# Kernel tuning notes

Hardware: AMD Instinct MI355X
Metric: run time of the kernel (lower is better)

The kernel has to match this reference:

```python
import jax, jax.numpy as jnp
import numpy as np

N = 50000      # num_nodes
E = 800000     # num_edges (avg degree 16)
D = 128        # embedding_dim
HID = 32       # per-head hidden dim of conv1
H = 8          # heads of conv1
OUT = 128      # output_dim


def setup_inputs() -> dict:
    key = jax.random.key(0)
    ks = jax.random.split(key, 14)
    s = lambda fan_in: 1.0 / np.sqrt(fan_in)
    return {
        "x": jax.random.randint(ks[0], (N,), 0, N),
        "edge_index": jax.random.randint(ks[1], (2, E), 0, N),
        "emb": jax.random.normal(ks[2], (N, D), jnp.float32),
        # conv1: GATConv(D, HID, heads=H, concat=True)
        "W1": jax.random.normal(ks[3], (D, H * HID), jnp.float32) * s(D),
        "a_src1": jax.random.normal(ks[4], (H, HID), jnp.float32) * s(HID),
        "a_dst1": jax.random.normal(ks[5], (H, HID), jnp.float32) * s(HID),
        "b1": jnp.zeros((H * HID,), jnp.float32),
        # conv2: GATConv(H*HID, OUT, heads=1, concat=False)
        "W2": jax.random.normal(ks[6], (H * HID, OUT), jnp.float32) * s(H * HID),
        "a_src2": jax.random.normal(ks[7], (1, OUT), jnp.float32) * s(OUT),
        "a_dst2": jax.random.normal(ks[8], (1, OUT), jnp.float32) * s(OUT),
        "b2": jnp.zeros((OUT,), jnp.float32),
        # output Linear(OUT, OUT)
        "Wo": jax.random.normal(ks[9], (OUT, OUT), jnp.float32) * s(OUT),
        "bo": jnp.zeros((OUT,), jnp.float32),
    }


def _segment_softmax(e, seg, n):
    # e: [E, H]; softmax over edges sharing the same destination node
    m = jax.ops.segment_max(e, seg, num_segments=n)            # [N, H]
    ex = jnp.exp(e - m[seg])
    denom = jax.ops.segment_sum(ex, seg, num_segments=n)       # [N, H]
    return ex / (denom[seg] + 1e-16)


def _gat_conv(x, src, dst, W, a_src, a_dst, b, concat):
    n = x.shape[0]
    Hh, C = a_src.shape
    h = (x @ W).reshape(n, Hh, C)                              # [N, H, C]
    al_src = (h * a_src).sum(-1)                               # [N, H]
    al_dst = (h * a_dst).sum(-1)                               # [N, H]
    e = jax.nn.leaky_relu(al_src[src] + al_dst[dst], 0.2)      # [E, H]
    alpha = _segment_softmax(e, dst, n)                        # [E, H]
    out = jax.ops.segment_sum(h[src] * alpha[:, :, None], dst, num_segments=n)
    out = out.reshape(n, Hh * C) if concat else out.mean(axis=1)
    return out + b


def reference(x, edge_index, emb, W1, a_src1, a_dst1, b1,
              W2, a_src2, a_dst2, b2, Wo, bo):
    n = x.shape[0]
    loops = jnp.arange(n)
    src = jnp.concatenate([edge_index[0], loops])              # add self-loops (PyG default)
    dst = jnp.concatenate([edge_index[1], loops])
    h = emb[x]                                                 # [N, D]
    h = _gat_conv(h, src, dst, W1, a_src1, a_dst1, b1, concat=True)
    h = _gat_conv(h, src, dst, W2, a_src2, a_dst2, b2, concat=False)
    return h @ Wo + bo
```

## Files before the change

kernel.cpp:

```cpp
#include <hip/hip_runtime.h>
#include <hip/hip_bf16.h>

#define NN 50000
#define EE 800000
#define DD 128
#define F1 256
#define F2 128

using short8  = __attribute__((ext_vector_type(8))) short;
using floatx4 = __attribute__((ext_vector_type(4))) float;

__device__ inline float bf2f(ushort u) { return __uint_as_float(((unsigned)u) << 16); }
__device__ inline ushort f2bf(float f) {
    unsigned u = __float_as_uint(f);
    u += 0x7fffu + ((u >> 16) & 1u);
    return (ushort)(u >> 16);
}

#define HB ((EE + 255) / 256)
#define W1B ((DD * F1 + 255) / 256)
#define W2B ((F1 * F2 + 255) / 256)
#define WOB ((F2 * F2 + 255) / 256)

__global__ __launch_bounds__(256) void k_prep(
    const int* __restrict__ edst, int* __restrict__ cnt,
    const float* __restrict__ W1, ushort* __restrict__ W1t,
    const float* __restrict__ W2, ushort* __restrict__ W2t,
    const float* __restrict__ Wo, ushort* __restrict__ Wot,
    const float* __restrict__ b2, const float* __restrict__ bo,
    float* __restrict__ bc) {
    int b = blockIdx.x;
    if (b < HB) {
        int i = b * 256 + threadIdx.x;
        if (i < EE) atomicAdd(&cnt[edst[i]], 1);
    } else if (b < HB + W1B) {
        int idx = (b - HB) * 256 + threadIdx.x;
        int k = idx / F1, n = idx % F1;
        W1t[(size_t)n * DD + k] = f2bf(W1[(size_t)k * F1 + n]);
    } else if (b < HB + W1B + W2B) {
        int idx = (b - HB - W1B) * 256 + threadIdx.x;
        int k = idx / F2, n = idx % F2;
        W2t[(size_t)n * F1 + k] = f2bf(W2[(size_t)k * F2 + n]);
    } else if (b < HB + W1B + W2B + WOB) {
        int idx = (b - HB - W1B - W2B) * 256 + threadIdx.x;
        int k = idx / F2, n = idx % F2;
        Wot[(size_t)n * F2 + k] = f2bf(Wo[(size_t)k * F2 + n]);
    } else {
        int j = threadIdx.x;
        if (j < F2) {
            float s = bo[j];
            for (int k = 0; k < F2; ++k) s += b2[k] * Wo[(size_t)k * F2 + j];
            bc[j] = s;
        }
    }
}

__global__ void k_scan1(const int* __restrict__ cnt, int* __restrict__ out,
                        int* __restrict__ sums) {
    __shared__ int s[256];
    int i = blockIdx.x * 256 + threadIdx.x;
    int v = (i < NN) ? cnt[i] + 1 : 0;
    s[threadIdx.x] = v;
    __syncthreads();
    for (int off = 1; off < 256; off <<= 1) {
        int t = (threadIdx.x >= off) ? s[threadIdx.x - off] : 0;
        __syncthreads();
        s[threadIdx.x] += t;
        __syncthreads();
    }
    if (i < NN) out[i] = s[threadIdx.x] - v;
    if (threadIdx.x == 255) sums[blockIdx.x] = s[255];
}

__global__ void k_scan3(int* __restrict__ offsets, const int* __restrict__ sums,
                        int* __restrict__ cursor, int nb) {
    __shared__ int s[256];
    int v = (threadIdx.x < nb) ? sums[threadIdx.x] : 0;
    s[threadIdx.x] = v;
    __syncthreads();
    for (int off = 1; off < 256; off <<= 1) {
        int t = (threadIdx.x >= off) ? s[threadIdx.x - off] : 0;
        __syncthreads();
        s[threadIdx.x] += t;
        __syncthreads();
    }
    int base = (blockIdx.x == 0) ? 0 : s[blockIdx.x - 1];
    int i = blockIdx.x * 256 + threadIdx.x;
    if (i < NN) {
        int o = offsets[i] + base;
        offsets[i] = o;
        cursor[i] = o;
    }
    if (blockIdx.x == 0 && threadIdx.x == 0) offsets[NN] = EE + NN;
}

__global__ void k_scatter(const int* __restrict__ esrc, const int* __restrict__ edst,
                          const int* __restrict__ offsets,
                          int* __restrict__ cursor, int* __restrict__ srcs) {
    int i = blockIdx.x * 256 + threadIdx.x;
    if (i < EE) {
        int pos = atomicAdd(&cursor[edst[i]], 1);
        srcs[pos] = esrc[i];
    } else if (i < EE + NN) {
        int n = i - EE;
        srcs[offsets[n + 1] - 1] = n;
    }
}

__global__ __launch_bounds__(256, 2) void k_gemm1(
    const int* __restrict__ x, const float* __restrict__ emb,
    const ushort* __restrict__ Bt,
    ushort* __restrict__ Cout,
    const float* __restrict__ avs, const float* __restrict__ avd,
    float* __restrict__ out_s, float* __restrict__ out_d) {
    __shared__ ushort As[128][72];
    __shared__ ushort Bs[128][72];
    const int t    = threadIdx.x;
    const int lane = t & 63;
    const int w    = t >> 6;
    const int wr   = w >> 1, wc = w & 1;
    const int m0   = blockIdx.x * 128;
    const int n0   = blockIdx.y * 128;
    floatx4 acc[4][4] = {};
    for (int k0 = 0; k0 < DD; k0 += 64) {
        #pragma unroll
        for (int p = 0; p < 4; ++p) {
            int linear = p * 2048 + t * 8;
            int row = linear >> 6;
            int col = linear & 63;
            short8 va = {};
            int gm = m0 + row;
            if (gm < NN) {
                const float* er = emb + (size_t)x[gm] * DD + k0 + col;
                float4 f0 = *(const float4*)er;
                float4 f1 = *(const float4*)(er + 4);
                va[0] = f2bf(f0.x); va[1] = f2bf(f0.y);
                va[2] = f2bf(f0.z); va[3] = f2bf(f0.w);
                va[4] = f2bf(f1.x); va[5] = f2bf(f1.y);
                va[6] = f2bf(f1.z); va[7] = f2bf(f1.w);
            }
            *(short8*)&As[row][col] = va;
            short8 vb = *(const short8*)(Bt + (size_t)(n0 + row) * DD + k0 + col);
            *(short8*)&Bs[row][col] = vb;
        }
        __syncthreads();
        #pragma unroll
        for (int kk = 0; kk < 64; kk += 32) {
            const int q8 = (lane >> 4) * 8;
            short8 af[4], bf[4];
            #pragma unroll
            for (int i = 0; i < 4; ++i)
                af[i] = *(const short8*)&As[wr * 64 + i * 16 + (lane & 15)][kk + q8];
            #pragma unroll
            for (int j = 0; j < 4; ++j)
                bf[j] = *(const short8*)&Bs[wc * 64 + j * 16 + (lane & 15)][kk + q8];
            #pragma unroll
            for (int i = 0; i < 4; ++i)
                #pragma unroll
                for (int j = 0; j < 4; ++j)
                    acc[i][j] = __builtin_amdgcn_mfma_f32_16x16x32_bf16(
                        af[i], bf[j], acc[i][j], 0, 0, 0);
        }
        __syncthreads();
    }
    const int r0 = (lane >> 4) * 4;
    const int cc = lane & 15;
    float as0 = avs[n0 + wc * 64 +  0 + cc], ad0 = avd[n0 + wc * 64 +  0 + cc];
    float as1 = avs[n0 + wc * 64 + 16 + cc], ad1 = avd[n0 + wc * 64 + 16 + cc];
    float as2 = avs[n0 + wc * 64 + 32 + cc], ad2 = avd[n0 + wc * 64 + 32 + cc];
    float as3 = avs[n0 + wc * 64 + 48 + cc], ad3 = avd[n0 + wc * 64 + 48 + cc];
    #pragma unroll
    for (int i = 0; i < 4; ++i) {
        #pragma unroll
        for (int r = 0; r < 4; ++r) {
            int m = m0 + wr * 64 + i * 16 + r0 + r;
            float hs0 = acc[i][0][r] * as0 + acc[i][1][r] * as1;
            float hs1 = acc[i][2][r] * as2 + acc[i][3][r] * as3;
            float hd0 = acc[i][0][r] * ad0 + acc[i][1][r] * ad1;
            float hd1 = acc[i][2][r] * ad2 + acc[i][3][r] * ad3;
            #pragma unroll
            for (int mask = 1; mask < 16; mask <<= 1) {
                hs0 += __shfl_xor(hs0, mask);
                hs1 += __shfl_xor(hs1, mask);
                hd0 += __shfl_xor(hd0, mask);
                hd1 += __shfl_xor(hd1, mask);
            }
            if (cc == 0 && m < NN) {
                int gh = (n0 >> 5) + wc * 2;
                out_s[m * 8 + gh] = hs0;   out_s[m * 8 + gh + 1] = hs1;
                out_d[m * 8 + gh] = hd0;   out_d[m * 8 + gh + 1] = hd1;
            }
            if (m < NN) {
                #pragma unroll
                for (int j = 0; j < 4; ++j)
                    Cout[(size_t)m * F1 + n0 + wc * 64 + j * 16 + cc] = f2bf(acc[i][j][r]);
            }
        }
    }
}

__global__ __launch_bounds__(256, 2) void k_gemm23(
    const ushort* __restrict__ A,
    const ushort* __restrict__ Bt,
    const ushort* __restrict__ Wot,
    ushort* __restrict__ h3,
    const float* __restrict__ avs, const float* __restrict__ avd,
    float* __restrict__ out_s, float* __restrict__ out_d) {
    __shared__ __align__(16) char smem[69632];
    ushort (*As)[72]   = (ushort(*)[72])smem;
    ushort (*Bs)[72]   = (ushort(*)[72])(smem + 18432);
    ushort (*h2t)[136] = (ushort(*)[136])smem;
    ushort (*Wt)[136]  = (ushort(*)[136])(smem + 34816);
    __shared__ float als[2][128], ald[2][128];
    const int t    = threadIdx.x;
    const int lane = t & 63;
    const int w    = t >> 6;
    const int wr   = w >> 1, wc = w & 1;
    const int m0   = blockIdx.x * 128;
    floatx4 acc[4][4] = {};
    for (int k0 = 0; k0 < F1; k0 += 64) {
        #pragma unroll
        for (int p = 0; p < 4; ++p) {
            int linear = p * 2048 + t * 8;
            int row = linear >> 6;
            int col = linear & 63;
            short8 va = {};
            int gm = m0 + row;
            if (gm < NN) va = *(const short8*)(A + (size_t)gm * F1 + k0 + col);
            *(short8*)&As[row][col] = va;
            short8 vb = *(const short8*)(Bt + (size_t)row * F1 + k0 + col);
            *(short8*)&Bs[row][col] = vb;
        }
        __syncthreads();
        #pragma unroll
        for (int kk = 0; kk < 64; kk += 32) {
            const int q8 = (lane >> 4) * 8;
            short8 af[4], bf[4];
            #pragma unroll
            for (int i = 0; i < 4; ++i)
                af[i] = *(const short8*)&As[wr * 64 + i * 16 + (lane & 15)][kk + q8];
            #pragma unroll
            for (int j = 0; j < 4; ++j)
                bf[j] = *(const short8*)&Bs[wc * 64 + j * 16 + (lane & 15)][kk + q8];
            #pragma unroll
            for (int i = 0; i < 4; ++i)
                #pragma unroll
                for (int j = 0; j < 4; ++j)
                    acc[i][j] = __builtin_amdgcn_mfma_f32_16x16x32_bf16(
                        af[i], bf[j], acc[i][j], 0, 0, 0);
        }
        __syncthreads();
    }
    const int r0 = (lane >> 4) * 4;
    const int cc = lane & 15;
    {
        float as0 = avs[wc * 64 +  0 + cc], ad0 = avd[wc * 64 +  0 + cc];
        float as1 = avs[wc * 64 + 16 + cc], ad1 = avd[wc * 64 + 16 + cc];
        float as2 = avs[wc * 64 + 32 + cc], ad2 = avd[wc * 64 + 32 + cc];
        float as3 = avs[wc * 64 + 48 + cc], ad3 = avd[wc * 64 + 48 + cc];
        #pragma unroll
        for (int i = 0; i < 4; ++i) {
            #pragma unroll
            for (int r = 0; r < 4; ++r) {
                float ps = acc[i][0][r] * as0 + acc[i][1][r] * as1
                         + acc[i][2][r] * as2 + acc[i][3][r] * as3;
                float pd = acc[i][0][r] * ad0 + acc[i][1][r] * ad1
                         + acc[i][2][r] * ad2 + acc[i][3][r] * ad3;
                #pragma unroll
                for (int mask = 1; mask < 16; mask <<= 1) {
                    ps += __shfl_xor(ps, mask);
                    pd += __shfl_xor(pd, mask);
                }
                if (cc == 0) {
                    int lr = wr * 64 + i * 16 + r0 + r;
                    als[wc][lr] = ps;
                    ald[wc][lr] = pd;
                }
            }
        }
    }
    #pragma unroll
    for (int i = 0; i < 4; ++i)
        #pragma unroll
        for (int r = 0; r < 4; ++r)
            #pragma unroll
            for (int j = 0; j < 4; ++j)
                h2t[wr * 64 + i * 16 + r0 + r][wc * 64 + j * 16 + cc] = f2bf(acc[i][j][r]);
    #pragma unroll
    for (int p = 0; p < 8; ++p) {
        int linear = p * 2048 + t * 8;
        int row = linear >> 7;
        int col = linear & 127;
        *(short8*)&Wt[row][col] = *(const short8*)(Wot + (size_t)row * F2 + col);
    }
    __syncthreads();
    if (t < 128) {
        int m = m0 + t;
        if (m < NN) {
            out_s[m] = als[0][t] + als[1][t];
            out_d[m] = ald[0][t] + ald[1][t];
        }
    }
    floatx4 acc2[4][4] = {};
    #pragma unroll
    for (int kk = 0; kk < 128; kk += 32) {
        const int q8 = (lane >> 4) * 8;
        short8 af[4], bf[4];
        #pragma unroll
        for (int i = 0; i < 4; ++i)
            af[i] = *(const short8*)&h2t[wr * 64 + i * 16 + (lane & 15)][kk + q8];
        #pragma unroll
        for (int j = 0; j < 4; ++j)
            bf[j] = *(const short8*)&Wt[wc * 64 + j * 16 + (lane & 15)][kk + q8];
        #pragma unroll
        for (int i = 0; i < 4; ++i)
            #pragma unroll
            for (int j = 0; j < 4; ++j)
                acc2[i][j] = __builtin_amdgcn_mfma_f32_16x16x32_bf16(
                    af[i], bf[j], acc2[i][j], 0, 0, 0);
    }
    #pragma unroll
    for (int i = 0; i < 4; ++i) {
        #pragma unroll
        for (int r = 0; r < 4; ++r) {
            int m = m0 + wr * 64 + i * 16 + r0 + r;
            if (m < NN) {
                #pragma unroll
                for (int j = 0; j < 4; ++j)
                    h3[(size_t)m * F2 + wc * 64 + j * 16 + cc] = f2bf(acc2[i][j][r]);
            }
        }
    }
}

__device__ inline float lrelu(float x) { return x > 0.f ? x : 0.2f * x; }

__global__ __launch_bounds__(256) void k_agg1(
    const int* __restrict__ offsets, const int* __restrict__ srcs,
    const ushort* __restrict__ h1, const float* __restrict__ a1s,
    const float* __restrict__ a1d, const float* __restrict__ b1,
    ushort* __restrict__ out1) {
    __shared__ float atab[4][512];
    __shared__ int   stab[4][64];
    const int w = threadIdx.x >> 6;
    const int d = blockIdx.x * 4 + w;
    if (d >= NN) return;
    const int lane = threadIdx.x & 63;
    const int beg = offsets[d], end = offsets[d + 1];
    const int deg = end - beg;
    const int e8 = lane >> 3, h8 = lane & 7;
    const float ad = a1d[d * 8 + h8];
    const int hh = lane >> 3;
    float4 acc = make_float4(0.f, 0.f, 0.f, 0.f);

    if (deg <= 64) {
        float m = -1e30f, den = 0.f;
        for (int e = e8; e < deg; e += 8) {
            int s = srcs[beg + e];
            if (h8 == 0) stab[w][e] = s;
            float v = lrelu(a1s[s * 8 + h8] + ad);
            atab[w][e * 8 + h8] = v;
            float nm = fmaxf(m, v);
            den = den * __expf(m - nm) + __expf(v - nm);
            m = nm;
        }
        #pragma unroll
        for (int mask = 8; mask < 64; mask <<= 1) {
            float om = __shfl_xor(m, mask);
            float od = __shfl_xor(den, mask);
            float nm = fmaxf(m, om);
            den = den * __expf(m - nm) + od * __expf(om - nm);
            m = nm;
        }
        float rden = 1.f / (den + 1e-16f);
        for (int p = lane; p < deg * 8; p += 64)
            atab[w][p] = __expf(atab[w][p] - m) * rden;
        int e = 0;
        for (; e + 8 <= deg; e += 8) {
            ushort4 u[8]; float a[8];
            #pragma unroll
            for (int jj = 0; jj < 8; ++jj) {
                int s = stab[w][e + jj];
                u[jj] = *(const ushort4*)(h1 + (size_t)s * F1 + lane * 4);
                a[jj] = atab[w][(e + jj) * 8 + hh];
            }
            #pragma unroll
            for (int jj = 0; jj < 8; ++jj) {
                acc.x += a[jj] * bf2f(u[jj].x);
                acc.y += a[jj] * bf2f(u[jj].y);
                acc.z += a[jj] * bf2f(u[jj].z);
                acc.w += a[jj] * bf2f(u[jj].w);
            }
        }
        for (; e < deg; ++e) {
            int s = stab[w][e];
            float alpha = atab[w][e * 8 + hh];
            ushort4 u = *(const ushort4*)(h1 + (size_t)s * F1 + lane * 4);
            acc.x += alpha * bf2f(u.x); acc.y += alpha * bf2f(u.y);
            acc.z += alpha * bf2f(u.z); acc.w += alpha * bf2f(u.w);
        }
    } else {
        float m = -1e30f, den = 0.f;
        for (int i = beg + e8; i < end; i += 8) {
            int s = srcs[i];
            float v = lrelu(a1s[s * 8 + h8] + ad);
            float nm = fmaxf(m, v);
            den = den * __expf(m - nm) + __expf(v - nm);
            m = nm;
        }
        #pragma unroll
        for (int mask = 8; mask < 64; mask <<= 1) {
            float om = __shfl_xor(m, mask);
            float od = __shfl_xor(den, mask);
            float nm = fmaxf(m, om);
            den = den * __expf(m - nm) + od * __expf(om - nm);
            m = nm;
        }
        float rden = 1.f / (den + 1e-16f);
        for (int tb = beg; tb < end; tb += 64) {
            int cnt = min(64, end - tb);
            if (lane < cnt) stab[w][lane] = srcs[tb + lane];
            int np = cnt * 8;
            for (int p = lane; p < np; p += 64) {
                int s = stab[w][p >> 3];
                float v = lrelu(a1s[s * 8 + h8] + ad);
                atab[w][p] = __expf(v - m) * rden;
            }
            for (int e = 0; e < cnt; ++e) {
                int s = stab[w][e];
                float alpha = atab[w][e * 8 + hh];
                ushort4 u = *(const ushort4*)(h1 + (size_t)s * F1 + lane * 4);
                acc.x += alpha * bf2f(u.x); acc.y += alpha * bf2f(u.y);
                acc.z += alpha * bf2f(u.z); acc.w += alpha * bf2f(u.w);
            }
        }
    }
    float4 bb = *(const float4*)(b1 + lane * 4);
    ushort4 o;
    o.x = f2bf(acc.x + bb.x); o.y = f2bf(acc.y + bb.y);
    o.z = f2bf(acc.z + bb.z); o.w = f2bf(acc.w + bb.w);
    *(ushort4*)(out1 + (size_t)d * F1 + lane * 4) = o;
}

__global__ __launch_bounds__(256) void k_agg2(
    const int* __restrict__ offsets, const int* __restrict__ srcs,
    const ushort* __restrict__ h3, const float* __restrict__ a2s,
    const float* __restrict__ a2d, const float* __restrict__ bc,
    float* __restrict__ out) {
    __shared__ float atab[4][64];
    __shared__ int   stab[4][64];
    const int w = threadIdx.x >> 6;
    const int d = blockIdx.x * 4 + w;
    if (d >= NN) return;
    const int lane = threadIdx.x & 63;
    const int beg = offsets[d], end = offsets[d + 1];
    const int deg = end - beg;
    const float ad = a2d[d];
    float2 acc = make_float2(0.f, 0.f);

    if (deg <= 64) {
        float m = -1e30f, den = 0.f;
        if (lane < deg) {
            int s = srcs[beg + lane];
            stab[w][lane] = s;
            float v = lrelu(a2s[s] + ad);
            atab[w][lane] = v;
            m = v;
            den = 1.f;
        }
        #pragma unroll
        for (int mask = 1; mask < 64; mask <<= 1) {
            float om = __shfl_xor(m, mask);
            float od = __shfl_xor(den, mask);
            float nm = fmaxf(m, om);
            den = den * __expf(m - nm) + od * __expf(om - nm);
            m = nm;
        }
        float rden = 1.f / (den + 1e-16f);
        if (lane < deg)
            atab[w][lane] = __expf(atab[w][lane] - m) * rden;
        int e = 0;
        for (; e + 8 <= deg; e += 8) {
            ushort2 u[8]; float a[8];
            #pragma unroll
            for (int jj = 0; jj < 8; ++jj) {
                int s = stab[w][e + jj];
                u[jj] = *(const ushort2*)(h3 + (size_t)s * F2 + lane * 2);
                a[jj] = atab[w][e + jj];
            }
            #pragma unroll
            for (int jj = 0; jj < 8; ++jj) {
                acc.x += a[jj] * bf2f(u[jj].x);
                acc.y += a[jj] * bf2f(u[jj].y);
            }
        }
        for (; e < deg; ++e) {
            int s = stab[w][e];
            float alpha = atab[w][e];
            ushort2 u = *(const ushort2*)(h3 + (size_t)s * F2 + lane * 2);
            acc.x += alpha * bf2f(u.x); acc.y += alpha * bf2f(u.y);
        }
    } else {
        float m = -1e30f, den = 0.f;
        for (int i = beg + lane; i < end; i += 64) {
            int s = srcs[i];
            float v = lrelu(a2s[s] + ad);
            float nm = fmaxf(m, v);
            den = den * __expf(m - nm) + __expf(v - nm);
            m = nm;
        }
        #pragma unroll
        for (int mask = 1; mask < 64; mask <<= 1) {
            float om = __shfl_xor(m, mask);
            float od = __shfl_xor(den, mask);
            float nm = fmaxf(m, om);
            den = den * __expf(m - nm) + od * __expf(om - nm);
            m = nm;
        }
        float rden = 1.f / (den + 1e-16f);
        for (int tb = beg; tb < end; tb += 64) {
            int cnt = min(64, end - tb);
            if (lane < cnt) {
                int s = srcs[tb + lane];
                stab[w][lane] = s;
                atab[w][lane] = __expf(lrelu(a2s[s] + ad) - m) * rden;
            }
            for (int e = 0; e < cnt; ++e) {
                int s = stab[w][e];
                float alpha = atab[w][e];
                ushort2 u = *(const ushort2*)(h3 + (size_t)s * F2 + lane * 2);
                acc.x += alpha * bf2f(u.x); acc.y += alpha * bf2f(u.y);
            }
        }
    }
    float2 bb = *(const float2*)(bc + lane * 2);
    *(float2*)(out + (size_t)d * F2 + lane * 2) = make_float2(acc.x + bb.x, acc.y + bb.y);
}

extern "C" void kernel_launch(void* const* d_in, const int* in_sizes, int n_in,
                              void* d_out, int out_size, void* d_ws, size_t ws_size,
                              hipStream_t stream) {
    const int*   x      = (const int*)d_in[0];
    const int*   edge   = (const int*)d_in[1];
    const float* emb    = (const float*)d_in[2];
    const float* W1     = (const float*)d_in[3];
    const float* a_src1 = (const float*)d_in[4];
    const float* a_dst1 = (const float*)d_in[5];
    const float* b1     = (const float*)d_in[6];
    const float* W2     = (const float*)d_in[7];
    const float* a_src2 = (const float*)d_in[8];
    const float* a_dst2 = (const float*)d_in[9];
    const float* b2     = (const float*)d_in[10];
    const float* Wo     = (const float*)d_in[11];
    const float* bo     = (const float*)d_in[12];
    float* out = (float*)d_out;

    char* w = (char*)d_ws;
    auto alloc = [&](size_t bytes) {
        char* p = w;
        w += (bytes + 255) & ~(size_t)255;
        return p;
    };
    int*    offsets = (int*)alloc((NN + 1) * sizeof(int));
    int*    cursor  = (int*)alloc(NN * sizeof(int));
    int*    sums    = (int*)alloc(256 * sizeof(int));
    int*    srcs    = (int*)alloc((size_t)(EE + NN) * sizeof(int));
    ushort* W1t     = (ushort*)alloc((size_t)DD * F1 * sizeof(ushort));
    ushort* W2t     = (ushort*)alloc((size_t)F1 * F2 * sizeof(ushort));
    ushort* Wot     = (ushort*)alloc((size_t)F2 * F2 * sizeof(ushort));
    ushort* h1      = (ushort*)alloc((size_t)NN * F1 * sizeof(ushort));
    ushort* out1    = (ushort*)alloc((size_t)NN * F1 * sizeof(ushort));
    ushort* h3      = (ushort*)alloc((size_t)NN * F2 * sizeof(ushort));
    float*  a1s     = (float*)alloc((size_t)NN * 8 * sizeof(float));
    float*  a1d     = (float*)alloc((size_t)NN * 8 * sizeof(float));
    float*  bc      = (float*)alloc(F2 * sizeof(float));
    float*  a2s     = a1s;
    float*  a2d     = a1d;

    const int* esrc = edge;
    const int* edst = edge + EE;

    const int NB = (NN + 255) / 256;

    hipMemsetAsync(cursor, 0, NN * sizeof(int), stream);
    k_prep<<<HB + W1B + W2B + WOB + 1, 256, 0, stream>>>(
        edst, cursor, W1, W1t, W2, W2t, Wo, Wot, b2, bo, bc);
    k_scan1<<<NB, 256, 0, stream>>>(cursor, offsets, sums);
    k_scan3<<<NB, 256, 0, stream>>>(offsets, sums, cursor, NB);
    k_scatter<<<(EE + NN + 255) / 256, 256, 0, stream>>>(esrc, edst, offsets, cursor, srcs);

    const int MT = (NN + 127) / 128;

    k_gemm1<<<dim3(MT, F1 / 128), 256, 0, stream>>>(
        x, emb, W1t, h1, a_src1, a_dst1, a1s, a1d);
    k_agg1<<<(NN + 3) / 4, 256, 0, stream>>>(offsets, srcs, h1, a1s, a1d, b1, out1);

    k_gemm23<<<dim3(MT, 1), 256, 0, stream>>>(
        out1, W2t, Wot, h3, a_src2, a_dst2, a2s, a2d);

    k_agg2<<<(NN + 3) / 4, 256, 0, stream>>>(offsets, srcs, h3, a2s, a2d, bc, out);
}
```

Baseline: 346.9 us.

## Fuse CSR build into cooperative kernel and use half-wave per node in aggregation

Replaces the memset plus the four preprocessing kernels (count, two scan passes, scatter) with a single cooperative kernel of 256 blocks that separates the phases with grid-wide syncs. This removes several launches and the memset, but the atomic count and scatter phases now run on only 256 blocks with grid-stride loops, where they used to run on thousands. Both aggregation kernels now give each destination node 32 lanes instead of a full 64-lane wavefront, with wider per-lane vector loads (8 bf16 in agg1, 4 in agg2) and 8 nodes per block. This is meant to cut idle lanes on low-degree nodes and raise memory-level parallelism for the gathers.

```diff
diff --git a/kernel.cpp b/kernel.cpp
--- a/kernel.cpp
+++ b/kernel.cpp
@@ -1,11 +1,15 @@
 #include <hip/hip_runtime.h>
 #include <hip/hip_bf16.h>
+#include <hip/hip_cooperative_groups.h>
+
+namespace cg = cooperative_groups;
 
 #define NN 50000
 #define EE 800000
 #define DD 128
 #define F1 256
 #define F2 128
+#define NB196 196
 
 using short8  = __attribute__((ext_vector_type(8))) short;
 using floatx4 = __attribute__((ext_vector_type(4))) float;
@@ -17,94 +21,87 @@
     return (ushort)(u >> 16);
 }
 
-#define HB ((EE + 255) / 256)
-#define W1B ((DD * F1 + 255) / 256)
-#define W2B ((F1 * F2 + 255) / 256)
-#define WOB ((F2 * F2 + 255) / 256)
-
-__global__ __launch_bounds__(256) void k_prep(
-    const int* __restrict__ edst, int* __restrict__ cnt,
+__global__ __launch_bounds__(256) void k_build(
+    const int* __restrict__ esrc, const int* __restrict__ edst,
+    int* __restrict__ cnt,
+    int* __restrict__ offsets, int* __restrict__ sums, int* __restrict__ srcs,
     const float* __restrict__ W1, ushort* __restrict__ W1t,
     const float* __restrict__ W2, ushort* __restrict__ W2t,
     const float* __restrict__ Wo, ushort* __restrict__ Wot,
     const float* __restrict__ b2, const float* __restrict__ bo,
     float* __restrict__ bc) {
-    int b = blockIdx.x;
-    if (b < HB) {
-        int i = b * 256 + threadIdx.x;
-        if (i < EE) atomicAdd(&cnt[edst[i]], 1);
-    } else if (b < HB + W1B) {
-        int idx = (b - HB) * 256 + threadIdx.x;
-        int k = idx / F1, n = idx % F1;
+    cg::grid_group grid = cg::this_grid();
+    const int tid = blockIdx.x * 256 + threadIdx.x;
+    const int NT  = gridDim.x * 256;
+    __shared__ int s[256];
+
+    for (int i = tid; i < NN; i += NT) cnt[i] = 0;
+    grid.sync();
+
+    for (int i = tid; i < EE; i += NT) atomicAdd(&cnt[edst[i]], 1);
+    for (int i = tid; i < DD * F1; i += NT) {
+        int k = i / F1, n = i % F1;
         W1t[(size_t)n * DD + k] = f2bf(W1[(size_t)k * F1 + n]);
-    } else if (b < HB + W1B + W2B) {
-        int idx = (b - HB - W1B) * 256 + threadIdx.x;
-        int k = idx / F2, n = idx % F2;
+    }
+    for (int i = tid; i < F1 * F2; i += NT) {
+        int k = i / F2, n = i % F2;
         W2t[(size_t)n * F1 + k] = f2bf(W2[(size_t)k * F2 + n]);
-    } else if (b < HB + W1B + W2B + WOB) {
-        int idx = (b - HB - W1B - W2B) * 256 + threadIdx.x;
-        int k = idx / F2, n = idx % F2;
+    }
+    for (int i = tid; i < F2 * F2; i += NT) {
+        int k = i / F2, n = i % F2;
         Wot[(size_t)n * F2 + k] = f2bf(Wo[(size_t)k * F2 + n]);
-    } else {
-        int j = threadIdx.x;
-        if (j < F2) {
-            float s = bo[j];
-            for (int k = 0; k < F2; ++k) s += b2[k] * Wo[(size_t)k * F2 + j];
-            bc[j] = s;
-        }
-    }
-}
-
-__global__ void k_scan1(const int* __restrict__ cnt, int* __restrict__ out,
-                        int* __restrict__ sums) {
-    __shared__ int s[256];
-    int i = blockIdx.x * 256 + threadIdx.x;
-    int v = (i < NN) ? cnt[i] + 1 : 0;
-    s[threadIdx.x] = v;
-    __syncthreads();
-    for (int off = 1; off < 256; off <<= 1) {
-        int t = (threadIdx.x >= off) ? s[threadIdx.x - off] : 0;
+    }
+    if (tid < F2) {
+        float acc = bo[tid];
+        for (int k = 0; k < F2; ++k) acc += b2[k] * Wo[(size_t)k * F2 + tid];
+        bc[tid] = acc;
+    }
+    grid.sync();
+
+    if (blockIdx.x < NB196) {
+        int i = blockIdx.x * 256 + threadIdx.x;
+        int v = (i < NN) ? cnt[i] + 1 : 0;
+        s[threadIdx.x] = v;
         __syncthreads();
-        s[threadIdx.x] += t;
+        for (int off = 1; off < 256; off <<= 1) {
+            int t2 = (threadIdx.x >= off) ? s[threadIdx.x - off] : 0;
+            __syncthreads();
+            s[threadIdx.x] += t2;
+            __syncthreads();
+        }
+        if (i < NN) offsets[i] = s[threadIdx.x] - v;
+        if (threadIdx.x == 255) sums[blockIdx.x] = s[255];
+    }
+    grid.sync();
+
+    {
+        int v = (threadIdx.x < NB196) ? sums[threadIdx.x] : 0;
+        s[threadIdx.x] = v;
         __syncthreads();
-    }
-    if (i < NN) out[i] = s[threadIdx.x] - v;
-    if (threadIdx.x == 255) sums[blockIdx.x] = s[255];
-}
-
-__global__ void k_scan3(int* __restrict__ offsets, const int* __restrict__ sums,
-                        int* __restrict__ cursor, int nb) {
-    __shared__ int s[256];
-    int v = (threadIdx.x < nb) ? sums[threadIdx.x] : 0;
-    s[threadIdx.x] = v;
-    __syncthreads();
-    for (int off = 1; off < 256; off <<= 1) {
-        int t = (threadIdx.x >= off) ? s[threadIdx.x - off] : 0;
-        __syncthreads();
-        s[threadIdx.x] += t;
-        __syncthreads();
-    }
-    int base = (blockIdx.x == 0) ? 0 : s[blockIdx.x - 1];
-    int i = blockIdx.x * 256 + threadIdx.x;
-    if (i < NN) {
-        int o = offsets[i] + base;
-        offsets[i] = o;
-        cursor[i] = o;
-    }
-    if (blockIdx.x == 0 && threadIdx.x == 0) offsets[NN] = EE + NN;
-}
-
-__global__ void k_scatter(const int* __restrict__ esrc, const int* __restrict__ edst,
-                          const int* __restrict__ offsets,
-                          int* __restrict__ cursor, int* __restrict__ srcs) {
-    int i = blockIdx.x * 256 + threadIdx.x;
-    if (i < EE) {
-        int pos = atomicAdd(&cursor[edst[i]], 1);
+        for (int off = 1; off < 256; off <<= 1) {
+            int t2 = (threadIdx.x >= off) ? s[threadIdx.x - off] : 0;
+            __syncthreads();
+            s[threadIdx.x] += t2;
+            __syncthreads();
+        }
+        if (blockIdx.x < NB196) {
+            int base = (blockIdx.x == 0) ? 0 : s[blockIdx.x - 1];
+            int i = blockIdx.x * 256 + threadIdx.x;
+            if (i < NN) {
+                int o = offsets[i] + base;
+                offsets[i] = o;
+                cnt[i] = o;
+            }
+        }
+        if (blockIdx.x == 0 && threadIdx.x == 0) offsets[NN] = EE + NN;
+    }
+    grid.sync();
+
+    for (int i = tid; i < EE; i += NT) {
+        int pos = atomicAdd(&cnt[edst[i]], 1);
         srcs[pos] = esrc[i];
-    } else if (i < EE + NN) {
-        int n = i - EE;
-        srcs[offsets[n + 1] - 1] = n;
-    }
+    }
+    for (int i = tid; i < NN; i += NT) srcs[offsets[i + 1] - 1] = i;
 }
 
 __global__ __launch_bounds__(256, 2) void k_gemm1(
@@ -340,32 +337,32 @@
     const ushort* __restrict__ h1, const float* __restrict__ a1s,
     const float* __restrict__ a1d, const float* __restrict__ b1,
     ushort* __restrict__ out1) {
-    __shared__ float atab[4][512];
-    __shared__ int   stab[4][64];
-    const int w = threadIdx.x >> 6;
-    const int d = blockIdx.x * 4 + w;
+    __shared__ float atab[8][512];
+    __shared__ int   stab[8][64];
+    const int hw = threadIdx.x >> 5;
+    const int d  = blockIdx.x * 8 + hw;
     if (d >= NN) return;
-    const int lane = threadIdx.x & 63;
+    const int l   = threadIdx.x & 31;
     const int beg = offsets[d], end = offsets[d + 1];
     const int deg = end - beg;
-    const int e8 = lane >> 3, h8 = lane & 7;
+    const int e4 = l >> 3, h8 = l & 7;
     const float ad = a1d[d * 8 + h8];
-    const int hh = lane >> 3;
-    float4 acc = make_float4(0.f, 0.f, 0.f, 0.f);
+    const int hh = l >> 2;
+    float accv[8] = {};
 
     if (deg <= 64) {
         float m = -1e30f, den = 0.f;
-        for (int e = e8; e < deg; e += 8) {
+        for (int e = e4; e < deg; e += 4) {
             int s = srcs[beg + e];
-            if (h8 == 0) stab[w][e] = s;
+            if (h8 == 0) stab[hw][e] = s;
             float v = lrelu(a1s[s * 8 + h8] + ad);
-            atab[w][e * 8 + h8] = v;
+            atab[hw][e * 8 + h8] = v;
             float nm = fmaxf(m, v);
             den = den * __expf(m - nm) + __expf(v - nm);
             m = nm;
         }
         #pragma unroll
-        for (int mask = 8; mask < 64; mask <<= 1) {
+        for (int mask = 8; mask < 32; mask <<= 1) {
             float om = __shfl_xor(m, mask);
             float od = __shfl_xor(den, mask);
             float nm = fmaxf(m, om);
@@ -373,35 +370,34 @@
             m = nm;
         }
         float rden = 1.f / (den + 1e-16f);
-        for (int p = lane; p < deg * 8; p += 64)
-            atab[w][p] = __expf(atab[w][p] - m) * rden;
+        for (int p = l; p < deg * 8; p += 32)
+            atab[hw][p] = __expf(atab[hw][p] - m) * rden;
         int e = 0;
-        for (; e + 8 <= deg; e += 8) {
-            ushort4 u[8]; float a[8];
-            #pragma unroll
-            for (int jj = 0; jj < 8; ++jj) {
-                int s = stab[w][e + jj];
-                u[jj] = *(const ushort4*)(h1 + (size_t)s * F1 + lane * 4);
-                a[jj] = atab[w][(e + jj) * 8 + hh];
-            }
-            #pragma unroll
-            for (int jj = 0; jj < 8; ++jj) {
-                acc.x += a[jj] * bf2f(u[jj].x);
-                acc.y += a[jj] * bf2f(u[jj].y);
-                acc.z += a[jj] * bf2f(u[jj].z);
-                acc.w += a[jj] * bf2f(u[jj].w);
-            }
+        for (; e + 4 <= deg; e += 4) {
+            short8 u[4]; float a[4];
+            #pragma unroll
+            for (int jj = 0; jj < 4; ++jj) {
+                int s = stab[hw][e + jj];
+                u[jj] = *(const short8*)(h1 + (size_t)s * F1 + l * 8);
+                a[jj] = atab[hw][(e + jj) * 8 + hh];
+            }
+            #pragma unroll
+            for (int jj = 0; jj < 4; ++jj)
+                #pragma unroll
+                for (int c = 0; c < 8; ++c)
+                    accv[c] += a[jj] * bf2f((ushort)u[jj][c]);
         }
         for (; e < deg; ++e) {
-            int s = stab[w][e];
-            float alpha = atab[w][e * 8 + hh];
-            ushort4 u = *(const ushort4*)(h1 + (size_t)s * F1 + lane * 4);
-            acc.x += alpha * bf2f(u.x); acc.y += alpha * bf2f(u.y);
-            acc.z += alpha * bf2f(u.z); acc.w += alpha * bf2f(u.w);
+            int s = stab[hw][e];
+            float alpha = atab[hw][e * 8 + hh];
+            short8 u = *(const short8*)(h1 + (size_t)s * F1 + l * 8);
+            #pragma unroll
+            for (int c = 0; c < 8; ++c)
+                accv[c] += alpha * bf2f((ushort)u[c]);
         }
     } else {
         float m = -1e30f, den = 0.f;
-        for (int i = beg + e8; i < end; i += 8) {
+        for (int i = beg + e4; i < end; i += 4) {
             int s = srcs[i];
             float v = lrelu(a1s[s * 8 + h8] + ad);
             float nm = fmaxf(m, v);
@@ -409,7 +405,7 @@
             m = nm;
         }
         #pragma unroll
-        for (int mask = 8; mask < 64; mask <<= 1) {
+        for (int mask = 8; mask < 32; mask <<= 1) {
             float om = __shfl_xor(m, mask);
             float od = __shfl_xor(den, mask);
             float nm = fmaxf(m, om);
@@ -419,27 +415,29 @@
         float rden = 1.f / (den + 1e-16f);
         for (int tb = beg; tb < end; tb += 64) {
             int cnt = min(64, end - tb);
-            if (lane < cnt) stab[w][lane] = srcs[tb + lane];
-            int np = cnt * 8;
-            for (int p = lane; p < np; p += 64) {
-                int s = stab[w][p >> 3];
-                float v = lrelu(a1s[s * 8 + h8] + ad);
-                atab[w][p] = __expf(v - m) * rden;
+            for (int e = l; e < cnt; e += 32) stab[hw][e] = srcs[tb + e];
+            for (int p = l; p < cnt * 8; p += 32) {
+                int s = stab[hw][p >> 3];
+                atab[hw][p] = __expf(lrelu(a1s[s * 8 + h8] + ad) - m) * rden;
             }
             for (int e = 0; e < cnt; ++e) {
-                int s = stab[w][e];
-                float alpha = atab[w][e * 8 + hh];
-                ushort4 u = *(const ushort4*)(h1 + (size_t)s * F1 + lane * 4);
-                acc.x += alpha * bf2f(u.x); acc.y += alpha * bf2f(u.y);
-                acc.z += alpha * bf2f(u.z); acc.w += alpha * bf2f(u.w);
-            }
-        }
-    }
-    float4 bb = *(const float4*)(b1 + lane * 4);
-    ushort4 o;
-    o.x = f2bf(acc.x + bb.x); o.y = f2bf(acc.y + bb.y);
-    o.z = f2bf(acc.z + bb.z); o.w = f2bf(acc.w + bb.w);
-    *(ushort4*)(out1 + (size_t)d * F1 + lane * 4) = o;
+                int s = stab[hw][e];
+                float alpha = atab[hw][e * 8 + hh];
+                short8 u = *(const short8*)(h1 + (size_t)s * F1 + l * 8);
+                #pragma unroll
+                for (int c = 0; c < 8; ++c)
+                    accv[c] += alpha * bf2f((ushort)u[c]);
+            }
+        }
+    }
+    float4 bb0 = *(const float4*)(b1 + l * 8);
+    float4 bb1 = *(const float4*)(b1 + l * 8 + 4);
+    short8 o;
+    o[0] = (short)f2bf(accv[0] + bb0.x); o[1] = (short)f2bf(accv[1] + bb0.y);
+    o[2] = (short)f2bf(accv[2] + bb0.z); o[3] = (short)f2bf(accv[3] + bb0.w);
+    o[4] = (short)f2bf(accv[4] + bb1.x); o[5] = (short)f2bf(accv[5] + bb1.y);
+    o[6] = (short)f2bf(accv[6] + bb1.z); o[7] = (short)f2bf(accv[7] + bb1.w);
+    *(short8*)(out1 + (size_t)d * F1 + l * 8) = o;
 }
 
 __global__ __launch_bounds__(256) void k_agg2(
@@ -447,29 +445,30 @@
     const ushort* __restrict__ h3, const float* __restrict__ a2s,
     const float* __restrict__ a2d, const float* __restrict__ bc,
     float* __restrict__ out) {
-    __shared__ float atab[4][64];
-    __shared__ int   stab[4][64];
-    const int w = threadIdx.x >> 6;
-    const int d = blockIdx.x * 4 + w;
+    __shared__ float atab[8][64];
+    __shared__ int   stab[8][64];
+    const int hw = threadIdx.x >> 5;
+    const int d  = blockIdx.x * 8 + hw;
     if (d >= NN) return;
-    const int lane = threadIdx.x & 63;
+    const int l   = threadIdx.x & 31;
     const int beg = offsets[d], end = offsets[d + 1];
     const int deg = end - beg;
     const float ad = a2d[d];
-    float2 acc = make_float2(0.f, 0.f);
+    float accv[4] = {};
 
     if (deg <= 64) {
         float m = -1e30f, den = 0.f;
-        if (lane < deg) {
-            int s = srcs[beg + lane];
-            stab[w][lane] = s;
+        for (int e = l; e < deg; e += 32) {
+            int s = srcs[beg + e];
+            stab[hw][e] = s;
             float v = lrelu(a2s[s] + ad);
-            atab[w][lane] = v;
-            m = v;
-            den = 1.f;
-        }
-        #pragma unroll
-        for (int mask = 1; mask < 64; mask <<= 1) {
+            atab[hw][e] = v;
+            float nm = fmaxf(m, v);
+            den = den * __expf(m - nm) + __expf(v - nm);
+            m = nm;
+        }
+        #pragma unroll
+        for (int mask = 1; mask < 32; mask <<= 1) {
             float om = __shfl_xor(m, mask);
             float od = __shfl_xor(den, mask);
             float nm = fmaxf(m, om);
@@ -477,32 +476,35 @@
             m = nm;
         }
         float rden = 1.f / (den + 1e-16f);
-        if (lane < deg)
-            atab[w][lane] = __expf(atab[w][lane] - m) * rden;
+        for (int p = l; p < deg; p += 32)
+            atab[hw][p] = __expf(atab[hw][p] - m) * rden;
         int e = 0;
         for (; e + 8 <= deg; e += 8) {
-            ushort2 u[8]; float a[8];
+            ushort4 u[8]; float a[8];
             #pragma unroll
             for (int jj = 0; jj < 8; ++jj) {
-                int s = stab[w][e + jj];
-                u[jj] = *(const ushort2*)(h3 + (size_t)s * F2 + lane * 2);
-                a[jj] = atab[w][e + jj];
+                int s = stab[hw][e + jj];
+                u[jj] = *(const ushort4*)(h3 + (size_t)s * F2 + l * 4);
+                a[jj] = atab[hw][e + jj];
             }
             #pragma unroll
             for (int jj = 0; jj < 8; ++jj) {
-                acc.x += a[jj] * bf2f(u[jj].x);
-                acc.y += a[jj] * bf2f(u[jj].y);
+                accv[0] += a[jj] * bf2f(u[jj].x);
+                accv[1] += a[jj] * bf2f(u[jj].y);
+                accv[2] += a[jj] * bf2f(u[jj].z);
+                accv[3] += a[jj] * bf2f(u[jj].w);
             }
         }
         for (; e < deg; ++e) {
-            int s = stab[w][e];
-            float alpha = atab[w][e];
-            ushort2 u = *(const ushort2*)(h3 + (size_t)s * F2 + lane * 2);
-            acc.x += alpha * bf2f(u.x); acc.y += alpha * bf2f(u.y);
+            int s = stab[hw][e];
+            float alpha = atab[hw][e];
+            ushort4 u = *(const ushort4*)(h3 + (size_t)s * F2 + l * 4);
+            accv[0] += alpha * bf2f(u.x); accv[1] += alpha * bf2f(u.y);
+            accv[2] += alpha * bf2f(u.z); accv[3] += alpha * bf2f(u.w);
         }
     } else {
         float m = -1e30f, den = 0.f;
-        for (int i = beg + lane; i < end; i += 64) {
+        for (int i = beg + l; i < end; i += 32) {
             int s = srcs[i];
             float v = lrelu(a2s[s] + ad);
             float nm = fmaxf(m, v);
@@ -510,7 +512,7 @@
             m = nm;
         }
         #pragma unroll
-        for (int mask = 1; mask < 64; mask <<= 1) {
+        for (int mask = 1; mask < 32; mask <<= 1) {
             float om = __shfl_xor(m, mask);
             float od = __shfl_xor(den, mask);
             float nm = fmaxf(m, om);
@@ -520,21 +522,23 @@
         float rden = 1.f / (den + 1e-16f);
         for (int tb = beg; tb < end; tb += 64) {
             int cnt = min(64, end - tb);
-            if (lane < cnt) {
-                int s = srcs[tb + lane];
-                stab[w][lane] = s;
-                atab[w][lane] = __expf(lrelu(a2s[s] + ad) - m) * rden;
+            for (int e = l; e < cnt; e += 32) {
+                int s = srcs[tb + e];
+                stab[hw][e] = s;
+                atab[hw][e] = __expf(lrelu(a2s[s] + ad) - m) * rden;
             }
             for (int e = 0; e < cnt; ++e) {
-                int s = stab[w][e];
-                float alpha = atab[w][e];
-                ushort2 u = *(const ushort2*)(h3 + (size_t)s * F2 + lane * 2);
-                acc.x += alpha * bf2f(u.x); acc.y += alpha * bf2f(u.y);
-            }
-        }
-    }
-    float2 bb = *(const float2*)(bc + lane * 2);
-    *(float2*)(out + (size_t)d * F2 + lane * 2) = make_float2(acc.x + bb.x, acc.y + bb.y);
+                int s = stab[hw][e];
+                float alpha = atab[hw][e];
+                ushort4 u = *(const ushort4*)(h3 + (size_t)s * F2 + l * 4);
+                accv[0] += alpha * bf2f(u.x); accv[1] += alpha * bf2f(u.y);
+                accv[2] += alpha * bf2f(u.z); accv[3] += alpha * bf2f(u.w);
+            }
+        }
+    }
+    float4 bb = *(const float4*)(bc + l * 4);
+    float4 o = make_float4(accv[0] + bb.x, accv[1] + bb.y, accv[2] + bb.z, accv[3] + bb.w);
+    *(float4*)(out + (size_t)d * F2 + l * 4) = o;
 }
 
 extern "C" void kernel_launch(void* const* d_in, const int* in_sizes, int n_in,
@@ -562,7 +566,7 @@
         return p;
     };
     int*    offsets = (int*)alloc((NN + 1) * sizeof(int));
-    int*    cursor  = (int*)alloc(NN * sizeof(int));
+    int*    cnt     = (int*)alloc(NN * sizeof(int));
     int*    sums    = (int*)alloc(256 * sizeof(int));
     int*    srcs    = (int*)alloc((size_t)(EE + NN) * sizeof(int));
     ushort* W1t     = (ushort*)alloc((size_t)DD * F1 * sizeof(ushort));
@@ -580,23 +584,23 @@
     const int* esrc = edge;
     const int* edst = edge + EE;
 
-    const int NB = (NN + 255) / 256;
-
-    hipMemsetAsync(cursor, 0, NN * sizeof(int), stream);
-    k_prep<<<HB + W1B + W2B + WOB + 1, 256, 0, stream>>>(
-        edst, cursor, W1, W1t, W2, W2t, Wo, Wot, b2, bo, bc);
-    k_scan1<<<NB, 256, 0, stream>>>(cursor, offsets, sums);
-    k_scan3<<<NB, 256, 0, stream>>>(offsets, sums, cursor, NB);
-    k_scatter<<<(EE + NN + 255) / 256, 256, 0, stream>>>(esrc, edst, offsets, cursor, srcs);
+    {
+        void* args[] = {
+            (void*)&esrc, (void*)&edst, (void*)&cnt, (void*)&offsets, (void*)&sums,
+            (void*)&srcs, (void*)&W1, (void*)&W1t, (void*)&W2, (void*)&W2t,
+            (void*)&Wo, (void*)&Wot, (void*)&b2, (void*)&bo, (void*)&bc
+        };
+        hipLaunchCooperativeKernel((void*)k_build, dim3(256), dim3(256), args, 0, stream);
+    }
 
     const int MT = (NN + 127) / 128;
 
     k_gemm1<<<dim3(MT, F1 / 128), 256, 0, stream>>>(
         x, emb, W1t, h1, a_src1, a_dst1, a1s, a1d);
-    k_agg1<<<(NN + 3) / 4, 256, 0, stream>>>(offsets, srcs, h1, a1s, a1d, b1, out1);
+    k_agg1<<<(NN + 7) / 8, 256, 0, stream>>>(offsets, srcs, h1, a1s, a1d, b1, out1);
 
     k_gemm23<<<dim3(MT, 1), 256, 0, stream>>>(
         out1, W2t, Wot, h3, a_src2, a_dst2, a2s, a2d);
 
-    k_agg2<<<(NN + 3) / 4, 256, 0, stream>>>(offsets, srcs, h3, a2s, a2d, bc, out);
+    k_agg2<<<(NN + 7) / 8, 256, 0, stream>>>(offsets, srcs, h3, a2s, a2d, bc, out);
 }
```

After: 463.9 us. +33.7%, slower.
